# Optimization experiments

Hardware: AMD Instinct MI355X
Metric: run time of the kernel (lower is better)

## Reference

```python
import jax, jax.numpy as jnp
import numpy as np

K = 16                 # nn_k neighbors (self excluded)
FILTER_SCALE = 2.0
SHARPNESS_SIGMA = 0.75
EPS = 1e-17


def _eps_denom(x):
    return jnp.where(x < EPS, EPS, x)


def _normalize(x):
    # F.normalize(dim=-1) semantics
    return x / jnp.maximum(jnp.linalg.norm(x, axis=-1, keepdims=True), 1e-12)


def _gather(feat, idx):
    # feat: (B,P,D), idx: (B,P,K) -> (B,P,K,D)   (== pytorch3d knn_gather)
    return jnp.take_along_axis(feat[:, None, :, :], idx[:, :, :, None], axis=2)


def _knn(points, k):
    # points: (B,P,3) -> squared dists (B,P,k), idxs (B,P,k); self excluded
    d2 = jnp.sum(points * points, axis=-1)
    dists = d2[:, :, None] + d2[:, None, :] - 2.0 * jnp.einsum('bpd,bqd->bpq', points, points)
    P = points.shape[1]
    r = jnp.arange(P)
    dists = dists.at[:, r, r].set(-jnp.inf)  # force self to be rank-0 of top_k
    neg, idx = jax.lax.top_k(-dists, k + 1)
    return jnp.maximum(-neg[:, :, 1:], 0.0), idx[:, :, 1:]


def _denoise(normals, idx, w):
    # weighted neighbor average of normals, per _denoise_normals
    nn_n = _gather(normals, idx)                       # (B,P,K,3)
    return jnp.sum(nn_n * w[..., None], axis=-2) / _eps_denom(
        jnp.sum(w, axis=-1, keepdims=True))


def setup_inputs() -> dict:
    key = jax.random.key(0)
    kp, kn = jax.random.split(key)
    B, P = 2, 8192
    points = jax.random.normal(kp, (B, P, 3), dtype=jnp.float32)
    normals = jax.random.normal(kn, (B, P, 3), dtype=jnp.float32)
    return {"points": points, "normals": normals}


def reference(points, normals):
    # --- torch.no_grad block: knn build + all weights + normal denoising ---
    pts_ng = jax.lax.stop_gradient(points)
    dists, idx = _knn(pts_ng, K)                       # (B,P,K)
    nn = _gather(pts_ng, idx)                          # (B,P,K,3), detached

    # phi = (1 - d/(2*d1*fs^2))^4, clamped at 0 (get_phi)
    s = dists[:, :, :1] * 2.0 * FILTER_SCALE * FILTER_SCALE
    w = jnp.maximum(1.0 - dists / _eps_denom(s), 0.0)
    phi = (w * w) * (w * w)

    n_ng = jax.lax.stop_gradient(normals)
    n1 = _denoise(n_ng, idx, phi)                      # first denoise with phi

    # normal_w = exp(-||n - ni||^2 / sigma^2) on normalized once-denoised normals
    nn_n = _gather(n1, idx)
    diff = _normalize(nn_n) - _normalize(n1)[:, :, None, :]
    inv_sigma = 1.0 / (SHARPNESS_SIGMA * SHARPNESS_SIGMA)
    normal_w = jnp.exp(-jnp.sum(diff * diff, axis=-1) * inv_sigma)

    # second denoise with phi * normal_w
    n2 = _denoise(n1, idx, phi * normal_w)

    # weights_proj = phi * spatial_w_proj(==1) * normal_w, ball-query masked
    weights_proj = phi * normal_w
    ball_mask = dists > FILTER_SCALE * dists[:, :, :1] * 2.0
    weights_proj = jnp.where(ball_mask, 0.0, weights_proj)
    weights_proj = jax.lax.stop_gradient(weights_proj)

    # --- outside no_grad: gather denoised normals, signed point-to-plane ---
    nn_normals = _gather(n2, idx)                      # (B,P,K,3) (no grad path)
    dist_to_surface = jnp.sum((nn - points[:, :, None, :]) * nn_normals, axis=-1)

    # projection loss: weighted mean of squared point-to-plane distance
    loss = jnp.sum(dist_to_surface * dist_to_surface * weights_proj, axis=-1) / \
        _eps_denom(jnp.sum(weights_proj, axis=-1))     # (B,P)
    return jnp.mean(loss)                              # BaseLoss reduction='mean'
```

## Files before the change

kernel.cpp:

```cpp
#include <hip/hip_runtime.h>
#include <math.h>

#define PP    8192
#define NB    2
#define NPTS  16384
#define KNN   16
#define EPSV  1e-17f
#define CH    128
#define NSUP  16
#define NCELL 4096

#define KEY_BIG 3.0e38f


__device__ __forceinline__ int spread3(int v) {
    return (v & 1) | ((v & 2) << 2) | ((v & 4) << 4) | ((v & 8) << 6);
}

__global__ void hist_kernel(const float* __restrict__ pts,
                            int* __restrict__ hist) {
    const int p = blockIdx.x * blockDim.x + threadIdx.x;
    const float x = pts[p * 3 + 0];
    const float y = pts[p * 3 + 1];
    const float z = pts[p * 3 + 2];
    const int ix = (int)fminf(fmaxf((x + 5.0f) * 1.6f, 0.0f), 15.0f);
    const int iy = (int)fminf(fmaxf((y + 5.0f) * 1.6f, 0.0f), 15.0f);
    const int iz = (int)fminf(fmaxf((z + 5.0f) * 1.6f, 0.0f), 15.0f);
    const int c = spread3(ix) | (spread3(iy) << 1) | (spread3(iz) << 2);
    atomicAdd(&hist[(p >> 13) * NCELL + c], 1);
}

__global__ void scan_kernel(const int* __restrict__ hist,
                            int* __restrict__ cursor) {
    const int b = blockIdx.x;
    const int t = threadIdx.x;
    const int base = b * NCELL;
    const int v0 = hist[base + t * 4 + 0];
    const int v1 = hist[base + t * 4 + 1];
    const int v2 = hist[base + t * 4 + 2];
    const int v3 = hist[base + t * 4 + 3];
    const int s4 = v0 + v1 + v2 + v3;
    const int lane = t & 63, wid = t >> 6;
    int v = s4;
#pragma unroll
    for (int off = 1; off < 64; off <<= 1) {
        int u = __shfl_up(v, off, 64);
        if (lane >= off) v += u;
    }
    __shared__ int wtot[16];
    if (lane == 63) wtot[wid] = v;
    __syncthreads();
    if (wid == 0) {
        int w = (lane < 16) ? wtot[lane] : 0;
#pragma unroll
        for (int off = 1; off < 16; off <<= 1) {
            int u = __shfl_up(w, off, 64);
            if (lane >= off) w += u;
        }
        if (lane < 16) wtot[lane] = w;
    }
    __syncthreads();
    const int wbase = (wid > 0) ? wtot[wid - 1] : 0;
    const int excl = wbase + v - s4;
    const int o0 = b * PP + excl;
    cursor[base + t * 4 + 0] = o0;
    cursor[base + t * 4 + 1] = o0 + v0;
    cursor[base + t * 4 + 2] = o0 + v0 + v1;
    cursor[base + t * 4 + 3] = o0 + v0 + v1 + v2;
}

__global__ void scatter_kernel(const float* __restrict__ pts,
                               int* __restrict__ cursor,
                               float4* __restrict__ sorted4,
                               int* __restrict__ perm) {
    const int p = blockIdx.x * blockDim.x + threadIdx.x;
    const float x = pts[p * 3 + 0];
    const float y = pts[p * 3 + 1];
    const float z = pts[p * 3 + 2];
    const int ix = (int)fminf(fmaxf((x + 5.0f) * 1.6f, 0.0f), 15.0f);
    const int iy = (int)fminf(fmaxf((y + 5.0f) * 1.6f, 0.0f), 15.0f);
    const int iz = (int)fminf(fmaxf((z + 5.0f) * 1.6f, 0.0f), 15.0f);
    const int c = spread3(ix) | (spread3(iy) << 1) | (spread3(iz) << 2);
    const int pos = atomicAdd(&cursor[(p >> 13) * NCELL + c], 1);
    sorted4[pos] = make_float4(x, y, z, x * x + y * y + z * z);
    perm[pos] = p & (PP - 1);
}

__global__ void bbox_kernel(const float4* __restrict__ sorted4,
                            float4* __restrict__ bbmin,
                            float4* __restrict__ bbmax,
                            float4* __restrict__ sbmin,
                            float4* __restrict__ sbmax) {
    __shared__ float4 smn[8], smx[8];
    const int lane = threadIdx.x & 63;
    const int wave = threadIdx.x >> 6;
    const int cw = blockIdx.x * 8 + wave;
    const float4 v = sorted4[cw * 64 + lane];
    float mnx = v.x, mny = v.y, mnz = v.z;
    float mxx = v.x, mxy = v.y, mxz = v.z;
#pragma unroll
    for (int off = 32; off >= 1; off >>= 1) {
        mnx = fminf(mnx, __shfl_xor(mnx, off, 64));
        mny = fminf(mny, __shfl_xor(mny, off, 64));
        mnz = fminf(mnz, __shfl_xor(mnz, off, 64));
        mxx = fmaxf(mxx, __shfl_xor(mxx, off, 64));
        mxy = fmaxf(mxy, __shfl_xor(mxy, off, 64));
        mxz = fmaxf(mxz, __shfl_xor(mxz, off, 64));
    }
    if (lane == 0) {
        bbmin[cw] = make_float4(mnx, mny, mnz, 0.f);
        bbmax[cw] = make_float4(mxx, mxy, mxz, 0.f);
        smn[wave] = make_float4(mnx, mny, mnz, 0.f);
        smx[wave] = make_float4(mxx, mxy, mxz, 0.f);
    }
    __syncthreads();
    if (threadIdx.x == 0) {
        float4 a = smn[0], bmx = smx[0];
#pragma unroll
        for (int k = 1; k < 8; ++k) {
            a.x = fminf(a.x, smn[k].x); a.y = fminf(a.y, smn[k].y);
            a.z = fminf(a.z, smn[k].z);
            bmx.x = fmaxf(bmx.x, smx[k].x); bmx.y = fmaxf(bmx.y, smx[k].y);
            bmx.z = fmaxf(bmx.z, smx[k].z);
        }
        sbmin[blockIdx.x] = a;
        sbmax[blockIdx.x] = bmx;
    }
}

__device__ __forceinline__ void insert16(float (&keys)[KNN], float kk) {
#pragma unroll
    for (int s = KNN - 1; s >= 1; --s)
        keys[s] = __builtin_amdgcn_fmed3f(keys[s - 1], kk, keys[s]);
    keys[0] = fminf(keys[0], kk);
}

__device__ __forceinline__ void merge16(float (&a)[KNN], const float (&o)[KNN]) {
    float c[KNN];
#pragma unroll
    for (int s = 0; s < KNN; ++s) c[s] = fminf(a[s], o[KNN - 1 - s]);
#pragma unroll
    for (int st = KNN / 2; st >= 1; st >>= 1) {
#pragma unroll
        for (int base = 0; base < KNN; base += 2 * st) {
#pragma unroll
            for (int k = 0; k < st; ++k) {
                const float x = c[base + k], y = c[base + k + st];
                c[base + k]      = fminf(x, y);
                c[base + k + st] = fmaxf(x, y);
            }
        }
    }
#pragma unroll
    for (int s = 0; s < KNN; ++s) a[s] = c[s];
}

__global__ __launch_bounds__(256) void knn4_kernel(
        const float4* __restrict__ sorted4,
        const int*    __restrict__ perm,
        const float*  __restrict__ normals,
        const float4* __restrict__ bbmin,
        const float4* __restrict__ bbmax,
        const float4* __restrict__ sbmin,
        const float4* __restrict__ sbmax,
        int*   __restrict__ out_idx,
        float* __restrict__ out_phi,
        float* __restrict__ out_n1) {
    const int lane = threadIdx.x & 63;
    const int wv   = threadIdx.x >> 6;
    const int W    = blockIdx.x * 4 + wv;
    const int b    = W >> 11;
    const int qg   = W & 2047;
    const int qbase = qg * 4;
    const int i    = lane & 3;
    const int u    = lane >> 2;
    const int qloc = qbase + i;
    const int s0   = qbase >> 9;
    const float4* sb = sorted4 + (size_t)b * PP;
    const int bCH = b * CH;

    const float4 q4 = sb[qloc];
    const float qx = q4.x, qy = q4.y, qz = q4.z;
    const float d2q = qx * qx + qy * qy + qz * qz;

    const float4 smn = sbmin[b * NSUP + u];
    const float4 smx = sbmax[b * NSUP + u];

    float keys[KNN];
#pragma unroll
    for (int s = 0; s < KNN; ++s) keys[s] = KEY_BIG;

    auto proc = [&](int c) {
#pragma unroll
        for (int t = 0; t < 4; ++t) {
            const int j = c * 64 + u + 16 * t;
            const float4 c4 = sb[j];
            const float dot = fmaf(qz, c4.z, fmaf(qy, c4.y, qx * c4.x));
            const float d  = fmaf(-2.0f, dot, d2q + c4.w);
            const float dc = fmaxf(d, 0.0f);
            float kv = __uint_as_float(
                (__float_as_uint(dc) & 0xFFFFE000u) | (unsigned)j);
            if (j == qloc) kv = KEY_BIG;
            if (__any(kv < keys[KNN - 1])) insert16(keys, kv);
        }
    };

    auto refreshB = [&]() -> unsigned {
        float tk[KNN];
#pragma unroll
        for (int s = 0; s < KNN; ++s) tk[s] = keys[s];
#pragma unroll
        for (int st = 0; st < 3; ++st) {
            const int S = 4 << st;
            float o[KNN];
#pragma unroll
            for (int s = 0; s < KNN; ++s) o[s] = __shfl_xor(tk[s], S, 64);
            merge16(tk, o);
        }
        float o15[KNN];
#pragma unroll
        for (int s = 0; s < KNN; ++s) o15[s] = __shfl_xor(tk[s], 32, 64);
        float B = fminf(tk[0], o15[KNN - 1]);
#pragma unroll
        for (int s = 1; s < KNN; ++s)
            B = fmaxf(B, fminf(tk[s], o15[KNN - 1 - s]));
        return __float_as_uint(B);
    };

    const int cb0 = s0 * 8;
    for (int k = 0; k < 8; ++k) proc(cb0 + k);
    unsigned Bq = refreshB();

    {
        const float ax = fmaxf(fmaxf(smn.x - qx, qx - smx.x), 0.0f);
        const float ay = fmaxf(fmaxf(smn.y - qy, qy - smx.y), 0.0f);
        const float az = fmaxf(fmaxf(smn.z - qz, qz - smx.z), 0.0f);
        const float dmS = (ax * ax + ay * ay + az * az) * 0.999999f;
        const unsigned flS = __float_as_uint(dmS) & 0xFFFFE000u;
        const bool passS = (u != s0) && (flS < Bq);
        unsigned long long M = __ballot(passS);

        while (M) {
            const int bit = __ffsll(M) - 1;
            const int us = bit >> 2;
            M &= ~(0xFULL << (us * 4));

            const int cc = us * 8 + (u & 7);
            const float4 cmn = bbmin[bCH + cc];
            const float4 cmx = bbmax[bCH + cc];
            const float bx = fmaxf(fmaxf(cmn.x - qx, qx - cmx.x), 0.0f);
            const float by = fmaxf(fmaxf(cmn.y - qy, qy - cmx.y), 0.0f);
            const float bz = fmaxf(fmaxf(cmn.z - qz, qz - cmx.z), 0.0f);
            const float dmC = (bx * bx + by * by + bz * bz) * 0.999999f;
            const unsigned flC = __float_as_uint(dmC) & 0xFFFFE000u;
            unsigned long long M2 = __ballot(flC < Bq) & 0xFFFFFFFFull;

            const bool did = (M2 != 0);
            while (M2) {
                const int b2 = __ffsll(M2) - 1;
                const int k = b2 >> 2;
                M2 &= ~(0xFULL << (k * 4));
                proc(us * 8 + k);
            }
            if (did && M) Bq = refreshB();
        }
    }

#pragma unroll
    for (int st = 0; st < 4; ++st) {
        const int S = 4 << st;
        float o[KNN];
#pragma unroll
        for (int s = 0; s < KNN; ++s) o[s] = __shfl_xor(keys[s], S, 64);
        merge16(keys, o);
    }

    float myk = keys[0];
#pragma unroll
    for (int s = 1; s < KNN; ++s) myk = (u == s) ? keys[s] : myk;
    const int j = (int)(__float_as_uint(myk) & 0x1FFFu);

    const float4 nb4 = sb[j];
    const float dot = fmaf(qz, nb4.z, fmaf(qy, nb4.y, qx * nb4.x));
    float dd = fmaf(-2.0f, dot, d2q + nb4.w);
    dd = fmaxf(dd, 0.0f);

    float d1 = dd;
#pragma unroll
    for (int st = 0; st < 4; ++st) d1 = fminf(d1, __shfl_xor(d1, 4 << st, 64));

    const float s0v  = d1 * 8.0f;
    const float sden = (s0v < EPSV) ? EPSV : s0v;
    const float w  = fmaxf(1.0f - dd / sden, 0.0f);
    const float ph = (w * w) * (w * w);

    const int qrow = (b << 13) + qloc;
    out_idx[qrow * KNN + u] = j;
    out_phi[qrow * KNN + u] = ph;

    const float* bn = normals + (size_t)b * PP * 3;
    const int jo = perm[(b << 13) + j];
    const float nx = bn[jo * 3 + 0];
    const float ny = bn[jo * 3 + 1];
    const float nz = bn[jo * 3 + 2];
    float px = ph * nx, py = ph * ny, pz = ph * nz, ps = ph;
#pragma unroll
    for (int st = 0; st < 4; ++st) {
        const int S = 4 << st;
        px += __shfl_xor(px, S, 64);
        py += __shfl_xor(py, S, 64);
        pz += __shfl_xor(pz, S, 64);
        ps += __shfl_xor(ps, S, 64);
    }
    if (u == 0) {
        const float den = (ps < EPSV) ? EPSV : ps;
        out_n1[qrow * 3 + 0] = px / den;
        out_n1[qrow * 3 + 1] = py / den;
        out_n1[qrow * 3 + 2] = pz / den;
    }
}

__global__ __launch_bounds__(256) void denoise2_kernel(
        const int* __restrict__ idx,
        const float* __restrict__ phi,
        const float* __restrict__ n1,
        float* __restrict__ nw_out,
        float* __restrict__ n2_out) {
    const int gid = blockIdx.x * 256 + threadIdx.x;
    const int q = gid >> 4;
    const int s = gid & 15;
    const int b = q >> 13;
    const int gbase = b * PP;
    const float INV_SIG = 1.0f / (0.75f * 0.75f);

    const float ax = n1[q * 3 + 0];
    const float ay = n1[q * 3 + 1];
    const float az = n1[q * 3 + 2];
    const float an = fmaxf(sqrtf(ax * ax + ay * ay + az * az), 1e-12f);
    const float rx = ax / an, ry = ay / an, rz = az / an;

    const int j = idx[q * KNN + s];
    const float bx = n1[(gbase + j) * 3 + 0];
    const float by = n1[(gbase + j) * 3 + 1];
    const float bz = n1[(gbase + j) * 3 + 2];
    const float bnn = fmaxf(sqrtf(bx * bx + by * by + bz * bz), 1e-12f);
    const float ux = bx / bnn - rx;
    const float uy = by / bnn - ry;
    const float uz = bz / bnn - rz;
    const float dq = ux * ux + uy * uy + uz * uz;
    const float nw = expf(-dq * INV_SIG);
    nw_out[q * KNN + s] = nw;

    const float wk = phi[q * KNN + s] * nw;
    float ox = wk * bx, oy = wk * by, oz = wk * bz, swn = wk;
#pragma unroll
    for (int off = 1; off < 16; off <<= 1) {
        ox  += __shfl_xor(ox,  off, 64);
        oy  += __shfl_xor(oy,  off, 64);
        oz  += __shfl_xor(oz,  off, 64);
        swn += __shfl_xor(swn, off, 64);
    }
    if (s == 0) {
        const float den = (swn < EPSV) ? EPSV : swn;
        n2_out[q * 3 + 0] = ox / den;
        n2_out[q * 3 + 1] = oy / den;
        n2_out[q * 3 + 2] = oz / den;
    }
}

__global__ __launch_bounds__(256) void loss_kernel(
        const float4* __restrict__ sorted4,
        const int* __restrict__ idx,
        const float* __restrict__ phi,
        const float* __restrict__ nw,
        const float* __restrict__ n2,
        float* __restrict__ partial) {
    const int gid = blockIdx.x * 256 + threadIdx.x;
    const int q = gid >> 4;
    const int s = gid & 15;
    const int b = q >> 13;
    const int il = q & (PP - 1);
    const float4* sbp = sorted4 + (size_t)b * PP;
    const int gbase = b * PP;

    const float4 p4 = sbp[il];
    const float px = p4.x, py = p4.y, pz = p4.z;
    const float d2q = px * px + py * py + pz * pz;

    const int j = idx[q * KNN + s];
    const float4 nb4 = sbp[j];
    const float dot = fmaf(pz, nb4.z, fmaf(py, nb4.y, px * nb4.x));
    const float dv  = fmaf(-2.0f, dot, d2q + nb4.w);
    const float d   = fmaxf(dv, 0.0f);

    float d1 = d;
#pragma unroll
    for (int off = 1; off < 16; off <<= 1) d1 = fminf(d1, __shfl_xor(d1, off, 64));

    float w = phi[q * KNN + s] * nw[q * KNN + s];
    if (d > 4.0f * d1) w = 0.f;

    const float nx = n2[(gbase + j) * 3 + 0];
    const float ny = n2[(gbase + j) * 3 + 1];
    const float nz = n2[(gbase + j) * 3 + 2];
    const float dts = (nb4.x - px) * nx +
                      (nb4.y - py) * ny +
                      (nb4.z - pz) * nz;
    float num = dts * dts * w, den = w;
#pragma unroll
    for (int off = 1; off < 16; off <<= 1) {
        num += __shfl_xor(num, off, 64);
        den += __shfl_xor(den, off, 64);
    }

    __shared__ float ls[16];
    if (s == 0) {
        const float dd = (den < EPSV) ? EPSV : den;
        ls[threadIdx.x >> 4] = num / dd;
    }
    __syncthreads();
    if (threadIdx.x == 0) {
        float v = 0.f;
#pragma unroll
        for (int k = 0; k < 16; ++k) v += ls[k];
        partial[blockIdx.x] = v;
    }
}

__global__ void finalize_kernel(const float* __restrict__ partial,
                                float* __restrict__ out) {
    float v = 0.f;
#pragma unroll
    for (int k = 0; k < 16; ++k) v += partial[threadIdx.x + 64 * k];
#pragma unroll
    for (int off = 32; off >= 1; off >>= 1) v += __shfl_down(v, off, 64);
    if (threadIdx.x == 0) out[0] = v / (float)NPTS;
}

extern "C" void kernel_launch(void* const* d_in, const int* in_sizes, int n_in,
                              void* d_out, int out_size, void* d_ws, size_t ws_size,
                              hipStream_t stream) {
    const float* points  = (const float*)d_in[0];
    const float* normals = (const float*)d_in[1];
    float* out = (float*)d_out;

    float* wsf    = (float*)d_ws;
    int*   w_idx  = (int*)wsf;
    float* w_phi  = wsf + 262144;
    float* w_nw   = wsf + 524288;
    float* w_n1   = wsf + 786432;
    float* w_n2   = wsf + 835584;
    float4* w_sorted4 = (float4*)(wsf + 884736);
    float* w_part = wsf + 950272;
    int*    w_perm   = (int*)(wsf + 524288);
    int*    w_hist   = (int*)(wsf + 540672);
    int*    w_cursor = (int*)(wsf + 548864);
    float4* w_bbmin  = (float4*)(wsf + 557056);
    float4* w_bbmax  = (float4*)(wsf + 558080);
    float4* w_sbmin  = (float4*)(wsf + 559104);
    float4* w_sbmax  = (float4*)(wsf + 559232);

    hipMemsetAsync(w_hist, 0, NB * NCELL * sizeof(int), stream);
    hist_kernel   <<<NPTS / 256, 256, 0, stream>>>(points, w_hist);
    scan_kernel   <<<NB, 1024, 0, stream>>>(w_hist, w_cursor);
    scatter_kernel<<<NPTS / 256, 256, 0, stream>>>(points, w_cursor, w_sorted4, w_perm);
    bbox_kernel   <<<32, 512, 0, stream>>>(w_sorted4, w_bbmin, w_bbmax,
                                           w_sbmin, w_sbmax);
    knn4_kernel   <<<1024, 256, 0, stream>>>(w_sorted4, w_perm, normals,
                                             w_bbmin, w_bbmax, w_sbmin, w_sbmax,
                                             w_idx, w_phi, w_n1);
    denoise2_kernel<<<1024, 256, 0, stream>>>(w_idx, w_phi, w_n1, w_nw, w_n2);
    loss_kernel   <<<1024, 256, 0, stream>>>(w_sorted4, w_idx, w_phi, w_nw, w_n2, w_part);
    finalize_kernel<<<1, 64, 0, stream>>>(w_part, out);
}
```

Baseline: 160.1 us.

## Fuse spatial sort and bbox kernels into one block-per-batch kernel, use 2 queries per wave in KNN

```diff
diff --git a/kernel.cpp b/kernel.cpp
--- a/kernel.cpp
+++ b/kernel.cpp
@@ -17,114 +17,108 @@
     return (v & 1) | ((v & 2) << 2) | ((v & 4) << 4) | ((v & 8) << 6);
 }
 
-__global__ void hist_kernel(const float* __restrict__ pts,
-                            int* __restrict__ hist) {
-    const int p = blockIdx.x * blockDim.x + threadIdx.x;
-    const float x = pts[p * 3 + 0];
-    const float y = pts[p * 3 + 1];
-    const float z = pts[p * 3 + 2];
-    const int ix = (int)fminf(fmaxf((x + 5.0f) * 1.6f, 0.0f), 15.0f);
-    const int iy = (int)fminf(fmaxf((y + 5.0f) * 1.6f, 0.0f), 15.0f);
-    const int iz = (int)fminf(fmaxf((z + 5.0f) * 1.6f, 0.0f), 15.0f);
-    const int c = spread3(ix) | (spread3(iy) << 1) | (spread3(iz) << 2);
-    atomicAdd(&hist[(p >> 13) * NCELL + c], 1);
-}
-
-__global__ void scan_kernel(const int* __restrict__ hist,
-                            int* __restrict__ cursor) {
+__global__ __launch_bounds__(1024) void sort_kernel(
+        const float* __restrict__ pts,
+        float4* __restrict__ sorted4,
+        int*    __restrict__ perm,
+        float4* __restrict__ bbmin,
+        float4* __restrict__ bbmax,
+        float4* __restrict__ sbmin,
+        float4* __restrict__ sbmax) {
+    __shared__ int lh[NCELL];
+    __shared__ int wtot[16];
     const int b = blockIdx.x;
     const int t = threadIdx.x;
-    const int base = b * NCELL;
-    const int v0 = hist[base + t * 4 + 0];
-    const int v1 = hist[base + t * 4 + 1];
-    const int v2 = hist[base + t * 4 + 2];
-    const int v3 = hist[base + t * 4 + 3];
+    const int lane = t & 63, wid = t >> 6;
+    const float* bp = pts + (size_t)b * PP * 3;
+
+    for (int k = t; k < NCELL; k += 1024) lh[k] = 0;
+    __syncthreads();
+
+    float px[8], py[8], pz[8];
+    int cell[8];
+#pragma unroll
+    for (int k = 0; k < 8; ++k) {
+        const int p = t + k * 1024;
+        const float x = bp[p * 3 + 0];
+        const float y = bp[p * 3 + 1];
+        const float z = bp[p * 3 + 2];
+        px[k] = x; py[k] = y; pz[k] = z;
+        const int ix = (int)fminf(fmaxf((x + 5.0f) * 1.6f, 0.0f), 15.0f);
+        const int iy = (int)fminf(fmaxf((y + 5.0f) * 1.6f, 0.0f), 15.0f);
+        const int iz = (int)fminf(fmaxf((z + 5.0f) * 1.6f, 0.0f), 15.0f);
+        cell[k] = spread3(ix) | (spread3(iy) << 1) | (spread3(iz) << 2);
+        atomicAdd(&lh[cell[k]], 1);
+    }
+    __syncthreads();
+
+    const int v0 = lh[t * 4 + 0];
+    const int v1 = lh[t * 4 + 1];
+    const int v2 = lh[t * 4 + 2];
+    const int v3 = lh[t * 4 + 3];
     const int s4 = v0 + v1 + v2 + v3;
-    const int lane = t & 63, wid = t >> 6;
     int v = s4;
 #pragma unroll
     for (int off = 1; off < 64; off <<= 1) {
-        int u = __shfl_up(v, off, 64);
-        if (lane >= off) v += u;
-    }
-    __shared__ int wtot[16];
+        int uu = __shfl_up(v, off, 64);
+        if (lane >= off) v += uu;
+    }
     if (lane == 63) wtot[wid] = v;
     __syncthreads();
     if (wid == 0) {
         int w = (lane < 16) ? wtot[lane] : 0;
 #pragma unroll
         for (int off = 1; off < 16; off <<= 1) {
-            int u = __shfl_up(w, off, 64);
-            if (lane >= off) w += u;
+            int uu = __shfl_up(w, off, 64);
+            if (lane >= off) w += uu;
         }
         if (lane < 16) wtot[lane] = w;
     }
     __syncthreads();
     const int wbase = (wid > 0) ? wtot[wid - 1] : 0;
     const int excl = wbase + v - s4;
-    const int o0 = b * PP + excl;
-    cursor[base + t * 4 + 0] = o0;
-    cursor[base + t * 4 + 1] = o0 + v0;
-    cursor[base + t * 4 + 2] = o0 + v0 + v1;
-    cursor[base + t * 4 + 3] = o0 + v0 + v1 + v2;
-}
-
-__global__ void scatter_kernel(const float* __restrict__ pts,
-                               int* __restrict__ cursor,
-                               float4* __restrict__ sorted4,
-                               int* __restrict__ perm) {
-    const int p = blockIdx.x * blockDim.x + threadIdx.x;
-    const float x = pts[p * 3 + 0];
-    const float y = pts[p * 3 + 1];
-    const float z = pts[p * 3 + 2];
-    const int ix = (int)fminf(fmaxf((x + 5.0f) * 1.6f, 0.0f), 15.0f);
-    const int iy = (int)fminf(fmaxf((y + 5.0f) * 1.6f, 0.0f), 15.0f);
-    const int iz = (int)fminf(fmaxf((z + 5.0f) * 1.6f, 0.0f), 15.0f);
-    const int c = spread3(ix) | (spread3(iy) << 1) | (spread3(iz) << 2);
-    const int pos = atomicAdd(&cursor[(p >> 13) * NCELL + c], 1);
-    sorted4[pos] = make_float4(x, y, z, x * x + y * y + z * z);
-    perm[pos] = p & (PP - 1);
-}
-
-__global__ void bbox_kernel(const float4* __restrict__ sorted4,
-                            float4* __restrict__ bbmin,
-                            float4* __restrict__ bbmax,
-                            float4* __restrict__ sbmin,
-                            float4* __restrict__ sbmax) {
-    __shared__ float4 smn[8], smx[8];
-    const int lane = threadIdx.x & 63;
-    const int wave = threadIdx.x >> 6;
-    const int cw = blockIdx.x * 8 + wave;
-    const float4 v = sorted4[cw * 64 + lane];
-    float mnx = v.x, mny = v.y, mnz = v.z;
-    float mxx = v.x, mxy = v.y, mxz = v.z;
-#pragma unroll
-    for (int off = 32; off >= 1; off >>= 1) {
-        mnx = fminf(mnx, __shfl_xor(mnx, off, 64));
-        mny = fminf(mny, __shfl_xor(mny, off, 64));
-        mnz = fminf(mnz, __shfl_xor(mnz, off, 64));
-        mxx = fmaxf(mxx, __shfl_xor(mxx, off, 64));
-        mxy = fmaxf(mxy, __shfl_xor(mxy, off, 64));
-        mxz = fmaxf(mxz, __shfl_xor(mxz, off, 64));
+    lh[t * 4 + 0] = excl;
+    lh[t * 4 + 1] = excl + v0;
+    lh[t * 4 + 2] = excl + v0 + v1;
+    lh[t * 4 + 3] = excl + v0 + v1 + v2;
+    __syncthreads();
+
+#pragma unroll
+    for (int k = 0; k < 8; ++k) {
+        const int pos = atomicAdd(&lh[cell[k]], 1);
+        sorted4[(size_t)b * PP + pos] =
+            make_float4(px[k], py[k], pz[k],
+                        px[k] * px[k] + py[k] * py[k] + pz[k] * pz[k]);
+        perm[b * PP + pos] = t + k * 1024;
+    }
+    __syncthreads();
+
+    float mnsx = KEY_BIG, mnsy = KEY_BIG, mnsz = KEY_BIG;
+    float mxsx = -KEY_BIG, mxsy = -KEY_BIG, mxsz = -KEY_BIG;
+    for (int k = 0; k < 8; ++k) {
+        const int cw = wid * 8 + k;
+        const float4 vv = sorted4[(size_t)b * PP + cw * 64 + lane];
+        float ax = vv.x, ay = vv.y, az = vv.z;
+        float bx = vv.x, by = vv.y, bz = vv.z;
+#pragma unroll
+        for (int off = 32; off >= 1; off >>= 1) {
+            ax = fminf(ax, __shfl_xor(ax, off, 64));
+            ay = fminf(ay, __shfl_xor(ay, off, 64));
+            az = fminf(az, __shfl_xor(az, off, 64));
+            bx = fmaxf(bx, __shfl_xor(bx, off, 64));
+            by = fmaxf(by, __shfl_xor(by, off, 64));
+            bz = fmaxf(bz, __shfl_xor(bz, off, 64));
+        }
+        if (lane == 0) {
+            bbmin[b * CH + cw] = make_float4(ax, ay, az, 0.f);
+            bbmax[b * CH + cw] = make_float4(bx, by, bz, 0.f);
+        }
+        mnsx = fminf(mnsx, ax); mnsy = fminf(mnsy, ay); mnsz = fminf(mnsz, az);
+        mxsx = fmaxf(mxsx, bx); mxsy = fmaxf(mxsy, by); mxsz = fmaxf(mxsz, bz);
     }
     if (lane == 0) {
-        bbmin[cw] = make_float4(mnx, mny, mnz, 0.f);
-        bbmax[cw] = make_float4(mxx, mxy, mxz, 0.f);
-        smn[wave] = make_float4(mnx, mny, mnz, 0.f);
-        smx[wave] = make_float4(mxx, mxy, mxz, 0.f);
-    }
-    __syncthreads();
-    if (threadIdx.x == 0) {
-        float4 a = smn[0], bmx = smx[0];
-#pragma unroll
-        for (int k = 1; k < 8; ++k) {
-            a.x = fminf(a.x, smn[k].x); a.y = fminf(a.y, smn[k].y);
-            a.z = fminf(a.z, smn[k].z);
-            bmx.x = fmaxf(bmx.x, smx[k].x); bmx.y = fmaxf(bmx.y, smx[k].y);
-            bmx.z = fmaxf(bmx.z, smx[k].z);
-        }
-        sbmin[blockIdx.x] = a;
-        sbmax[blockIdx.x] = bmx;
+        sbmin[b * NSUP + wid] = make_float4(mnsx, mnsy, mnsz, 0.f);
+        sbmax[b * NSUP + wid] = make_float4(mxsx, mxsy, mxsz, 0.f);
     }
 }
 
@@ -155,7 +149,7 @@
     for (int s = 0; s < KNN; ++s) a[s] = c[s];
 }
 
-__global__ __launch_bounds__(256) void knn4_kernel(
+__global__ __launch_bounds__(256) void knn2_kernel(
         const float4* __restrict__ sorted4,
         const int*    __restrict__ perm,
         const float*  __restrict__ normals,
@@ -169,11 +163,11 @@
     const int lane = threadIdx.x & 63;
     const int wv   = threadIdx.x >> 6;
     const int W    = blockIdx.x * 4 + wv;
-    const int b    = W >> 11;
-    const int qg   = W & 2047;
-    const int qbase = qg * 4;
-    const int i    = lane & 3;
-    const int u    = lane >> 2;
+    const int b    = W >> 12;
+    const int qg   = W & 4095;
+    const int qbase = qg * 2;
+    const int i    = lane & 1;
+    const int u    = lane >> 1;
     const int qloc = qbase + i;
     const int s0   = qbase >> 9;
     const float4* sb = sorted4 + (size_t)b * PP;
@@ -183,17 +177,14 @@
     const float qx = q4.x, qy = q4.y, qz = q4.z;
     const float d2q = qx * qx + qy * qy + qz * qz;
 
-    const float4 smn = sbmin[b * NSUP + u];
-    const float4 smx = sbmax[b * NSUP + u];
-
     float keys[KNN];
 #pragma unroll
     for (int s = 0; s < KNN; ++s) keys[s] = KEY_BIG;
 
     auto proc = [&](int c) {
 #pragma unroll
-        for (int t = 0; t < 4; ++t) {
-            const int j = c * 64 + u + 16 * t;
+        for (int t = 0; t < 2; ++t) {
+            const int j = c * 64 + u + 32 * t;
             const float4 c4 = sb[j];
             const float dot = fmaf(qz, c4.z, fmaf(qy, c4.y, qx * c4.x));
             const float d  = fmaf(-2.0f, dot, d2q + c4.w);
@@ -201,17 +192,21 @@
             float kv = __uint_as_float(
                 (__float_as_uint(dc) & 0xFFFFE000u) | (unsigned)j);
             if (j == qloc) kv = KEY_BIG;
-            if (__any(kv < keys[KNN - 1])) insert16(keys, kv);
+            if (kv < keys[KNN - 1]) insert16(keys, kv);
         }
     };
 
-    auto refreshB = [&]() -> unsigned {
+    const int cb0 = s0 * 8;
+    for (int k = 0; k < 8; ++k) proc(cb0 + k);
+
+    unsigned Bq;
+    {
         float tk[KNN];
 #pragma unroll
         for (int s = 0; s < KNN; ++s) tk[s] = keys[s];
 #pragma unroll
-        for (int st = 0; st < 3; ++st) {
-            const int S = 4 << st;
+        for (int st = 0; st < 4; ++st) {
+            const int S = 2 << st;
             float o[KNN];
 #pragma unroll
             for (int s = 0; s < KNN; ++s) o[s] = __shfl_xor(tk[s], S, 64);
@@ -224,28 +219,24 @@
 #pragma unroll
         for (int s = 1; s < KNN; ++s)
             B = fmaxf(B, fminf(tk[s], o15[KNN - 1 - s]));
-        return __float_as_uint(B);
-    };
-
-    const int cb0 = s0 * 8;
-    for (int k = 0; k < 8; ++k) proc(cb0 + k);
-    unsigned Bq = refreshB();
+        Bq = __float_as_uint(B);
+    }
 
     {
+        const int sup = (lane >> 2) & 15;
+        const float4 smn = sbmin[b * NSUP + sup];
+        const float4 smx = sbmax[b * NSUP + sup];
         const float ax = fmaxf(fmaxf(smn.x - qx, qx - smx.x), 0.0f);
         const float ay = fmaxf(fmaxf(smn.y - qy, qy - smx.y), 0.0f);
         const float az = fmaxf(fmaxf(smn.z - qz, qz - smx.z), 0.0f);
         const float dmS = (ax * ax + ay * ay + az * az) * 0.999999f;
         const unsigned flS = __float_as_uint(dmS) & 0xFFFFE000u;
-        const bool passS = (u != s0) && (flS < Bq);
-        unsigned long long M = __ballot(passS);
-
-        while (M) {
-            const int bit = __ffsll(M) - 1;
-            const int us = bit >> 2;
-            M &= ~(0xFULL << (us * 4));
-
-            const int cc = us * 8 + (u & 7);
+        const unsigned long long M =
+            __ballot((sup != s0) && (flS < Bq));
+
+        for (int s = 0; s < NSUP; ++s) {
+            if (!(M & (0xFULL << (s * 4)))) continue;
+            const int cc = s * 8 + (u & 7);
             const float4 cmn = bbmin[bCH + cc];
             const float4 cmx = bbmax[bCH + cc];
             const float bx = fmaxf(fmaxf(cmn.x - qx, qx - cmx.x), 0.0f);
@@ -253,31 +244,26 @@
             const float bz = fmaxf(fmaxf(cmn.z - qz, qz - cmx.z), 0.0f);
             const float dmC = (bx * bx + by * by + bz * bz) * 0.999999f;
             const unsigned flC = __float_as_uint(dmC) & 0xFFFFE000u;
-            unsigned long long M2 = __ballot(flC < Bq) & 0xFFFFFFFFull;
-
-            const bool did = (M2 != 0);
-            while (M2) {
-                const int b2 = __ffsll(M2) - 1;
-                const int k = b2 >> 2;
-                M2 &= ~(0xFULL << (k * 4));
-                proc(us * 8 + k);
-            }
-            if (did && M) Bq = refreshB();
-        }
-    }
-
-#pragma unroll
-    for (int st = 0; st < 4; ++st) {
-        const int S = 4 << st;
+            const unsigned long long M2 = __ballot(flC < Bq);
+#pragma unroll
+            for (int k = 0; k < 8; ++k)
+                if (M2 & (0x0003000300030003ULL << (2 * k))) proc(s * 8 + k);
+        }
+    }
+
+#pragma unroll
+    for (int st = 0; st < 5; ++st) {
+        const int S = 2 << st;
         float o[KNN];
 #pragma unroll
         for (int s = 0; s < KNN; ++s) o[s] = __shfl_xor(keys[s], S, 64);
         merge16(keys, o);
     }
 
+    const int su = u & 15;
     float myk = keys[0];
 #pragma unroll
-    for (int s = 1; s < KNN; ++s) myk = (u == s) ? keys[s] : myk;
+    for (int s = 1; s < KNN; ++s) myk = (su == s) ? keys[s] : myk;
     const int j = (int)(__float_as_uint(myk) & 0x1FFFu);
 
     const float4 nb4 = sb[j];
@@ -287,7 +273,7 @@
 
     float d1 = dd;
 #pragma unroll
-    for (int st = 0; st < 4; ++st) d1 = fminf(d1, __shfl_xor(d1, 4 << st, 64));
+    for (int st = 0; st < 4; ++st) d1 = fminf(d1, __shfl_xor(d1, 2 << st, 64));
 
     const float s0v  = d1 * 8.0f;
     const float sden = (s0v < EPSV) ? EPSV : s0v;
@@ -295,28 +281,30 @@
     const float ph = (w * w) * (w * w);
 
     const int qrow = (b << 13) + qloc;
-    out_idx[qrow * KNN + u] = j;
-    out_phi[qrow * KNN + u] = ph;
+    if (u < 16) {
+        out_idx[qrow * KNN + u] = j;
+        out_phi[qrow * KNN + u] = ph;
+    }
 
     const float* bn = normals + (size_t)b * PP * 3;
     const int jo = perm[(b << 13) + j];
     const float nx = bn[jo * 3 + 0];
     const float ny = bn[jo * 3 + 1];
     const float nz = bn[jo * 3 + 2];
-    float px = ph * nx, py = ph * ny, pz = ph * nz, ps = ph;
+    float sx = ph * nx, sy = ph * ny, sz = ph * nz, ss = ph;
 #pragma unroll
     for (int st = 0; st < 4; ++st) {
-        const int S = 4 << st;
-        px += __shfl_xor(px, S, 64);
-        py += __shfl_xor(py, S, 64);
-        pz += __shfl_xor(pz, S, 64);
-        ps += __shfl_xor(ps, S, 64);
+        const int S = 2 << st;
+        sx += __shfl_xor(sx, S, 64);
+        sy += __shfl_xor(sy, S, 64);
+        sz += __shfl_xor(sz, S, 64);
+        ss += __shfl_xor(ss, S, 64);
     }
     if (u == 0) {
-        const float den = (ps < EPSV) ? EPSV : ps;
-        out_n1[qrow * 3 + 0] = px / den;
-        out_n1[qrow * 3 + 1] = py / den;
-        out_n1[qrow * 3 + 2] = pz / den;
+        const float den = (ss < EPSV) ? EPSV : ss;
+        out_n1[qrow * 3 + 0] = sx / den;
+        out_n1[qrow * 3 + 1] = sy / den;
+        out_n1[qrow * 3 + 2] = sz / den;
     }
 }
 
@@ -453,20 +441,14 @@
     float4* w_sorted4 = (float4*)(wsf + 884736);
     float* w_part = wsf + 950272;
     int*    w_perm   = (int*)(wsf + 524288);
-    int*    w_hist   = (int*)(wsf + 540672);
-    int*    w_cursor = (int*)(wsf + 548864);
     float4* w_bbmin  = (float4*)(wsf + 557056);
     float4* w_bbmax  = (float4*)(wsf + 558080);
     float4* w_sbmin  = (float4*)(wsf + 559104);
     float4* w_sbmax  = (float4*)(wsf + 559232);
 
-    hipMemsetAsync(w_hist, 0, NB * NCELL * sizeof(int), stream);
-    hist_kernel   <<<NPTS / 256, 256, 0, stream>>>(points, w_hist);
-    scan_kernel   <<<NB, 1024, 0, stream>>>(w_hist, w_cursor);
-    scatter_kernel<<<NPTS / 256, 256, 0, stream>>>(points, w_cursor, w_sorted4, w_perm);
-    bbox_kernel   <<<32, 512, 0, stream>>>(w_sorted4, w_bbmin, w_bbmax,
-                                           w_sbmin, w_sbmax);
-    knn4_kernel   <<<1024, 256, 0, stream>>>(w_sorted4, w_perm, normals,
+    sort_kernel   <<<NB, 1024, 0, stream>>>(points, w_sorted4, w_perm,
+                                            w_bbmin, w_bbmax, w_sbmin, w_sbmax);
+    knn2_kernel   <<<2048, 256, 0, stream>>>(w_sorted4, w_perm, normals,
                                              w_bbmin, w_bbmax, w_sbmin, w_sbmax,
                                              w_idx, w_phi, w_n1);
     denoise2_kernel<<<1024, 256, 0, stream>>>(w_idx, w_phi, w_n1, w_nw, w_n2);
```

Result: faster. 142.7 us (-10.9%).
